# Optimization experiments

Measured on AMD Instinct MI355X. Metric: run time of the kernel, lower is better.

Reference implementation:

```python
import jax, jax.numpy as jnp
import numpy as np

B, N = 2, 1024
DIM, HEADS, DH, MLP = 768, 12, 64, 3072
PD = 768          # channels * patch_size^2 = 3*16*16
GRID = 16         # image_size // patch_size
DEPTH = 8
INNER = HEADS * DH


def layer_norm(x, g):
    # torch F.layer_norm with beta=0 buffer, eps=1e-5
    m = x.mean(-1, keepdims=True)
    v = ((x - m) ** 2).mean(-1, keepdims=True)
    return (x - m) / jnp.sqrt(v + 1e-5) * g


def qk_rmsnorm(x, g):
    # F.normalize(x, dim=-1) * sqrt(DH) * gamma ; gamma is [H,1,DH]
    n = jnp.linalg.norm(x, axis=-1, keepdims=True)
    return x / jnp.maximum(n, 1e-12) * (DH ** 0.5) * g


def setup_inputs() -> dict:
    key = jax.random.key(0)
    ks = jax.random.split(key, 16)
    s = 0.02
    d = {
        "patches": jax.random.normal(ks[0], (B, N, PD), dtype=jnp.float32),
        "h_idx": jax.random.randint(ks[1], (B, N), 0, GRID),
        "w_idx": jax.random.randint(ks[2], (B, N), 0, GRID),
        "image_ids": jnp.sort(jax.random.randint(ks[3], (B, N), 0, 8), axis=-1),
        "pos_h": jax.random.normal(ks[4], (GRID, PD)) * s,
        "pos_w": jax.random.normal(ks[5], (GRID, PD)) * s,
        "Wp": jax.random.normal(ks[6], (PD, DIM)) * s,
        "bp": jnp.zeros((DIM,)),
        "ln_p": jnp.ones((DIM,)),
        "ln1": jnp.ones((DEPTH, DIM)),
        "qg": jnp.ones((DEPTH, HEADS, 1, DH)),
        "kg": jnp.ones((DEPTH, HEADS, 1, DH)),
        "Wq": jax.random.normal(ks[7], (DEPTH, DIM, INNER)) * s,
        "Wkv": jax.random.normal(ks[8], (DEPTH, DIM, 2 * INNER)) * s,
        "Wo": jax.random.normal(ks[9], (DEPTH, INNER, DIM)) * s,
        "ln2": jnp.ones((DEPTH, DIM)),
        "W1": jax.random.normal(ks[10], (DEPTH, DIM, MLP)) * s,
        "b1": jnp.zeros((DEPTH, MLP)),
        "W2": jax.random.normal(ks[11], (DEPTH, MLP, DIM)) * s,
        "b2": jnp.zeros((DEPTH, DIM)),
        "lnf": jnp.ones((DIM,)),
    }
    return d


def reference(patches, h_idx, w_idx, image_ids, pos_h, pos_w, Wp, bp, ln_p,
              ln1, qg, kg, Wq, Wkv, Wo, ln2, W1, b1, W2, b2, lnf):
    # pos embed added to raw patches before projection (pos_embed_before_proj=True)
    x = patches + pos_h[h_idx] + pos_w[w_idx]            # [B,N,PD]
    x = layer_norm(x @ Wp + bp, ln_p)                    # [B,N,DIM]

    # block-diagonal attn_mask: tokens attend only within their own packed image
    mask = image_ids[:, None, :, None] == image_ids[:, None, None, :]  # [B,1,N,N]

    for i in range(DEPTH):
        xn = layer_norm(x, ln1[i])
        q = (xn @ Wq[i]).reshape(B, N, HEADS, DH).transpose(0, 2, 1, 3)
        k, v = jnp.split(xn @ Wkv[i], 2, axis=-1)
        k = k.reshape(B, N, HEADS, DH).transpose(0, 2, 1, 3)
        v = v.reshape(B, N, HEADS, DH).transpose(0, 2, 1, 3)
        q = qk_rmsnorm(q, qg[i])
        k = qk_rmsnorm(k, kg[i])
        dots = jnp.einsum('bhid,bhjd->bhij', q, k)       # [B,H,N,N]
        dots = jnp.where(mask, dots, -jnp.finfo(dots.dtype).max)
        attn = jax.nn.softmax(dots, axis=-1)
        o = jnp.einsum('bhij,bhjd->bhid', attn, v)
        o = o.transpose(0, 2, 1, 3).reshape(B, N, INNER)
        x = o @ Wo[i] + x
        h = jax.nn.gelu(layer_norm(x, ln2[i]) @ W1[i] + b1[i], approximate=False)
        x = (h @ W2[i] + b2[i]) + x
    return layer_norm(x, lnf)
```

## Files before the change

kernel.cpp:

```cpp
#include <hip/hip_runtime.h>
#include <hip/hip_bf16.h>
#include <math.h>

typedef _Float16 f16;
typedef f16   f16x8 __attribute__((ext_vector_type(8)));
typedef float f32x4 __attribute__((ext_vector_type(4)));
typedef unsigned short ushort_t;

#define DIM   768
#define HEADS 12
#define DH    64
#define MLP_  3072
#define NTOK  2048
#define SEQ   1024
#define WELTS 7077888

__device__ __forceinline__ ushort_t h2u(f16 h){ return __builtin_bit_cast(ushort_t, h); }
__device__ __forceinline__ unsigned pk2h(float a, float b){
  return (unsigned)h2u((f16)a) | ((unsigned)h2u((f16)b) << 16);
}
__device__ __forceinline__ void gload16(const void* g, void* l){
  __builtin_amdgcn_global_load_lds(
      (const __attribute__((address_space(1))) void*)g,
      (__attribute__((address_space(3))) void*)l, 16, 0, 0);
}
__device__ __forceinline__ float wred_sum(float v){
  #pragma unroll
  for (int o = 32; o > 0; o >>= 1) v += __shfl_xor(v, o);
  return v;
}

__global__ __launch_bounds__(256) void convert_w_kernel(
    const float* __restrict__ Wq, const float* __restrict__ Wkv,
    const float* __restrict__ Wo, const float* __restrict__ W1,
    const float* __restrict__ W2, int layer, int wp_only,
    f16* __restrict__ th)
{
  int bid = blockIdx.x;
  const float* src; int K, N; size_t ooff; int t;
  if (wp_only){ src = Wq; K = 768; N = 768; ooff = 0; t = bid; }
  else if (bid < 288) { src = Wq;  K = 768;  N = 768;  ooff = 0;       t = bid; }
  else if (bid < 864) { src = Wkv; K = 768;  N = 1536; ooff = 589824;  t = bid - 288; }
  else if (bid < 1152){ src = Wo;  K = 768;  N = 768;  ooff = 1769472; t = bid - 864; }
  else if (bid < 2304){ src = W1;  K = 768;  N = 3072; ooff = 2359296; t = bid - 1152; }
  else                { src = W2;  K = 3072; N = 768;  ooff = 4718592; t = bid - 2304; }
  if (!wp_only) src += (size_t)layer * K * N;
  int ntn = N >> 6;
  int tk = t / ntn, tn = t % ntn;
  int k0 = tk * 32, n0 = tn * 64;

  __shared__ ushort_t lh[32][66];
  int tid = threadIdx.x;
  #pragma unroll
  for (int rr = 0; rr < 2; rr++){
    int k = rr * 16 + (tid >> 4);
    int n = (tid & 15) * 4;
    float4 v = *(const float4*)(src + (size_t)(k0 + k) * N + n0 + n);
    lh[k][n+0] = h2u((f16)v.x); lh[k][n+1] = h2u((f16)v.y);
    lh[k][n+2] = h2u((f16)v.z); lh[k][n+3] = h2u((f16)v.w);
  }
  __syncthreads();
  int n = tid >> 2, kq = tid & 3;
  unsigned ph[4];
  #pragma unroll
  for (int j = 0; j < 4; j++)
    ph[j] = (unsigned)lh[kq*8 + 2*j][n] | ((unsigned)lh[kq*8 + 2*j + 1][n] << 16);
  size_t obase = ooff + (size_t)(n0 + n) * K + k0 + kq * 8;
  *(uint4*)(th + obase) = make_uint4(ph[0], ph[1], ph[2], ph[3]);
}

template<int MW>
__global__ __launch_bounds__(256) void gemm_kernel(
    const f16* __restrict__ Aq, const f16* __restrict__ Bw,
    const float* __restrict__ bias, const float* __restrict__ res,
    float* __restrict__ C, f16* __restrict__ Cq,
    f16* __restrict__ Qh, f16* __restrict__ Kt, f16* __restrict__ Vt,
    int N, int K, int nbx, int mode)
{
  constexpr int BM = MW * 32;
  __shared__ __align__(16) f16 sA[2][BM * 64];
  __shared__ __align__(16) f16 sB[2][64 * 64];
  const int tid = threadIdx.x;
  const int wid = tid >> 6, lane = tid & 63;
  constexpr int nbyl = (MW == 4) ? 4 : 5;
  const int nwg = nbx << nbyl;
  const int bid = blockIdx.x;
  const int swz = (bid & 7) * (nwg >> 3) + (bid >> 3);
  const int by = swz & ((1 << nbyl) - 1), bx = swz >> nbyl;
  const int brow = by * BM, bcol = bx << 6;
  const int m2 = wid & 1, n2 = wid >> 1;
  const int fr = lane & 15, fq = lane >> 4;
  const int Kc = K / (int)gridDim.z;
  const int kbase = (int)blockIdx.z * Kc;
  const int nk = Kc >> 6;

  const f16* pA = Aq + (size_t)brow * K + kbase;
  const f16* pB = Bw + (size_t)bcol * K + kbase;

  f32x4 acc[MW][2] = {};

  auto STAGE = [&](int buf, int ks){
    const int k0 = ks << 6;
    #pragma unroll
    for (int i = 0; i < MW; i++){
      int idx = tid + i * 256;
      int r = idx >> 3, c = idx & 7;
      int gc = c ^ (r & 7);
      gload16(pA + (size_t)r * K + k0 + gc * 8, &sA[buf][idx * 8]);
    }
    #pragma unroll
    for (int i = 0; i < 2; i++){
      int idx = tid + i * 256;
      int r = idx >> 3, c = idx & 7;
      int gc = c ^ (r & 7);
      gload16(pB + (size_t)r * K + k0 + gc * 8, &sB[buf][idx * 8]);
    }
  };

  STAGE(0, 0);
  __syncthreads();
  int cur = 0;
  for (int ks = 0; ks < nk; ks++){
    if (ks + 1 < nk) STAGE(cur ^ 1, ks + 1);
    #pragma unroll
    for (int s = 0; s < 2; s++){
      f16x8 a[MW], b[2];
      #pragma unroll
      for (int m = 0; m < MW; m++){
        int r = m2 * (MW * 16) + m * 16 + fr;
        int ch = (s * 4 + fq) ^ (r & 7);
        a[m] = *(const f16x8*)(&sA[cur][r * 64 + ch * 8]);
      }
      #pragma unroll
      for (int n = 0; n < 2; n++){
        int r = n2 * 32 + n * 16 + fr;
        int ch = (s * 4 + fq) ^ (r & 7);
        b[n] = *(const f16x8*)(&sB[cur][r * 64 + ch * 8]);
      }
      #pragma unroll
      for (int m = 0; m < MW; m++)
        #pragma unroll
        for (int n = 0; n < 2; n++)
          acc[m][n] = __builtin_amdgcn_mfma_f32_16x16x32_f16(a[m], b[n], acc[m][n], 0, 0, 0);
    }
    __syncthreads();
    cur ^= 1;
  }

  #pragma unroll
  for (int n = 0; n < 2; n++){
    int col = bcol + n2 * 32 + n * 16 + fr;
    float bv = bias ? bias[col] : 0.f;
    #pragma unroll
    for (int m = 0; m < MW; m++){
      int row0 = brow + m2 * (MW * 16) + m * 16 + (fq << 2);
      if (mode == 3){
        float* P = C + (size_t)blockIdx.z * ((size_t)NTOK * N);
        #pragma unroll
        for (int i = 0; i < 4; i++)
          P[(size_t)(row0 + i) * N + col] = acc[m][n][i];
      } else if (mode == 2){
        if (col < 768){
          #pragma unroll
          for (int i = 0; i < 4; i++)
            Qh[(size_t)(row0 + i) * 768 + col] = (f16)acc[m][n][i];
        } else if (col < 1536){
          int hcol = col - 768, hh = hcol >> 6, dd = hcol & 63;
          #pragma unroll
          for (int i = 0; i < 4; i++){
            int row = row0 + i;
            int bq = row >> 10, tok = row & 1023;
            Kt[((size_t)(bq * 12 + hh) * 1024 + tok) * 64 + dd] = (f16)acc[m][n][i];
          }
        } else {
          int hcol = col - 1536, hh = hcol >> 6, dd = hcol & 63;
          int bq = row0 >> 10, tok0 = row0 & 1023;
          ushort4 sv;
          sv.x = h2u((f16)acc[m][n][0]); sv.y = h2u((f16)acc[m][n][1]);
          sv.z = h2u((f16)acc[m][n][2]); sv.w = h2u((f16)acc[m][n][3]);
          *(ushort4*)(Vt + ((size_t)((bq * 12 + hh) * 64 + dd)) * 1024 + tok0) = sv;
        }
      } else if (mode == 1){
        #pragma unroll
        for (int i = 0; i < 4; i++){
          float v = acc[m][n][i] + bv;
          float ge = 0.5f * v * (1.f + erff(v * 0.70710678118654752f));
          Cq[(size_t)(row0 + i) * N + col] = (f16)ge;
        }
      } else {
        #pragma unroll
        for (int i = 0; i < 4; i++){
          float v = acc[m][n][i] + bv;
          size_t o = (size_t)(row0 + i) * N + col;
          if (res) v += res[o];
          C[o] = v;
        }
      }
    }
  }
}

__global__ __launch_bounds__(256) void lnred_kernel(
    float* __restrict__ x, const float* __restrict__ p, const float* __restrict__ badd,
    const float* __restrict__ g, f16* __restrict__ yq, float* __restrict__ yf)
{
  int wid = threadIdx.x >> 6, lane = threadIdx.x & 63;
  int row = blockIdx.x * 4 + wid;
  float* xr = x + (size_t)row * DIM;
  float v[12]; float s = 0.f;
  if (p){
    const float* p0 = p + (size_t)row * DIM;
    const float* p1 = p0 + (size_t)NTOK * DIM;
    #pragma unroll
    for (int d = 0; d < 12; d++){
      int c = d * 64 + lane;
      float t = xr[c] + p0[c] + p1[c] + badd[c];
      xr[c] = t; v[d] = t; s += t;
    }
  } else {
    #pragma unroll
    for (int d = 0; d < 12; d++){ v[d] = xr[d * 64 + lane]; s += v[d]; }
  }
  s = wred_sum(s);
  float mean = s * (1.f / 768.f);
  float q2 = 0.f;
  #pragma unroll
  for (int d = 0; d < 12; d++){ float t = v[d] - mean; q2 += t * t; }
  q2 = wred_sum(q2);
  float rstd = rsqrtf(q2 * (1.f / 768.f) + 1e-5f);
  size_t base = (size_t)row * DIM;
  #pragma unroll
  for (int d = 0; d < 12; d++){
    float y = (v[d] - mean) * rstd * g[d * 64 + lane];
    if (yq) yq[base + d * 64 + lane] = (f16)y;
    else    yf[base + d * 64 + lane] = y;
  }
}

__global__ __launch_bounds__(256) void rms_kernel(
    f16* __restrict__ qh, f16* __restrict__ kt,
    const float* __restrict__ qg, const float* __restrict__ kg)
{
  int wid = threadIdx.x >> 6, lane = threadIdx.x & 63;
  int id = blockIdx.x * 4 + wid;
  f16* p; const float* g;
  if (id < 24576){
    int tok = id / HEADS, h = id % HEADS;
    p = qh + (size_t)tok * DIM + h * 64; g = qg + h * 64;
  } else {
    int id2 = id - 24576;
    p = kt + (size_t)id2 * 64; g = kg + ((id2 >> 10) % 12) * 64;
  }
  float v = (float)p[lane];
  float n2 = wred_sum(v * v);
  float nn = fmaxf(sqrtf(n2), 1e-12f);
  p[lane] = (f16)(v * (8.f / nn) * g[lane]);
}

__global__ __launch_bounds__(256) void posadd_kernel(
    const float* __restrict__ patches, const int* __restrict__ hi,
    const int* __restrict__ wi, const float* __restrict__ ph,
    const float* __restrict__ pw, f16* __restrict__ oq)
{
  int idx = blockIdx.x * 256 + threadIdx.x;
  int tok = idx / 192, cv = idx % 192;
  float4 p = ((const float4*)patches)[idx];
  float4 a = *(const float4*)(ph + (size_t)hi[tok] * DIM + cv * 4);
  float4 b = *(const float4*)(pw + (size_t)wi[tok] * DIM + cv * 4);
  ushort4 o;
  o.x = h2u((f16)(p.x + a.x + b.x)); o.y = h2u((f16)(p.y + a.y + b.y));
  o.z = h2u((f16)(p.z + a.z + b.z)); o.w = h2u((f16)(p.w + a.w + b.w));
  ((ushort4*)oq)[idx] = o;
}

__global__ void seg_kernel(const int* __restrict__ ids, int2* __restrict__ segs)
{
  int i = blockIdx.x * 256 + threadIdx.x;
  int b = blockIdx.y;
  const int* row = ids + b * SEQ;
  int v = row[i];
  int lo = 0, hi = SEQ;
  while (lo < hi){ int mid = (lo + hi) >> 1; if (row[mid] <  v) lo = mid + 1; else hi = mid; }
  int s = lo;
  lo = 0; hi = SEQ;
  while (lo < hi){ int mid = (lo + hi) >> 1; if (row[mid] <= v) lo = mid + 1; else hi = mid; }
  segs[b * SEQ + i] = make_int2(s, lo);
}

__global__ __launch_bounds__(256) void attn_kernel(
    const f16* __restrict__ qh, const f16* __restrict__ ktp,
    const f16* __restrict__ vt, const int2* __restrict__ segs,
    f16* __restrict__ oq)
{
  __shared__ __align__(16) ushort_t Kq[32 * 64];
  __shared__ __align__(16) ushort_t Vl[64 * 40];

  const int tid = threadIdx.x;
  const int w = tid >> 6, lane = tid & 63;
  const int q15 = lane & 15, kg = lane >> 4;
  const int bh = blockIdx.x, b = bh / 12, h = bh % 12;
  const int qt = blockIdx.y;
  const int qrow = qt * 64 + w * 16 + q15;
  const size_t qtok = (size_t)b * SEQ + qrow;

  const f16* qp = qh + qtok * DIM + h * 64 + kg * 8;
  f16x8 qf[2];
  qf[0] = *(const f16x8*)(qp);
  qf[1] = *(const f16x8*)(qp + 32);

  const int2 se  = segs[qtok];
  const int2 se0 = segs[(size_t)b * SEQ + qt * 64];
  const int2 se1 = segs[(size_t)b * SEQ + qt * 64 + 63];
  const int klo = se0.x & ~31, khi = se1.y;

  float m = -3.0e38f, l = 0.f;
  f32x4 oacc[4] = {};

  const int krl = tid >> 3, kcl = tid & 7;
  const int kgc = kcl ^ (krl & 7);
  const f16* kbase = ktp + (size_t)bh * 1024 * 64;
  const int vd = tid >> 2, vko = (tid & 3) * 8;

  for (int kt0 = klo; kt0 < khi; kt0 += 32){
    gload16(kbase + (size_t)(kt0 + krl) * 64 + kgc * 8, Kq + tid * 8);
    {
      int ksrc = kt0 + vko;
      uint4 vv = *(const uint4*)(vt + ((size_t)bh * 64 + vd) * SEQ + ksrc);
      *(uint4*)((char*)Vl + vd * 80 + vko * 2) = vv;
    }
    __syncthreads();

    f32x4 s[2] = {};
    #pragma unroll
    for (int dh2 = 0; dh2 < 2; dh2++){
      #pragma unroll
      for (int khf = 0; khf < 2; khf++){
        int row = khf * 16 + q15;
        unsigned off = ((unsigned)row << 7) + ((unsigned)(dh2 * 4 + kg) << 4);
        off ^= (unsigned)(row & 7) << 4;
        f16x8 kf = *(const f16x8*)((const char*)Kq + off);
        s[khf] = __builtin_amdgcn_mfma_f32_16x16x32_f16(kf, qf[dh2], s[khf], 0, 0, 0);
      }
    }

    float p[8]; float tmax = -3.0e38f;
    #pragma unroll
    for (int khf = 0; khf < 2; khf++)
      #pragma unroll
      for (int i = 0; i < 4; i++){
        int key = kt0 + khf * 16 + kg * 4 + i;
        bool val = (key >= se.x) && (key < se.y);
        float sv = val ? s[khf][i] : -3.0e38f;
        p[khf * 4 + i] = sv;
        tmax = fmaxf(tmax, sv);
      }
    tmax = fmaxf(tmax, __shfl_xor(tmax, 16));
    tmax = fmaxf(tmax, __shfl_xor(tmax, 32));
    float mnew = fmaxf(m, tmax);
    float sc = __expf(m - mnew);
    float psum = 0.f;
    #pragma unroll
    for (int j = 0; j < 8; j++){
      float pv = (p[j] > -1.0e38f) ? __expf(p[j] - mnew) : 0.f;
      p[j] = pv; psum += pv;
    }
    psum += __shfl_xor(psum, 16);
    psum += __shfl_xor(psum, 32);
    l = l * sc + psum;
    m = mnew;
    #pragma unroll
    for (int dt = 0; dt < 4; dt++) oacc[dt] *= sc;

    unsigned u00 = pk2h(p[0], p[1]), u01 = pk2h(p[2], p[3]);
    unsigned u10 = pk2h(p[4], p[5]), u11 = pk2h(p[6], p[7]);
    int s0l = q15 + ((kg & 1) << 5);
    int s1l = s0l + 16;
    unsigned a0 = __shfl(u00, s0l), b0 = __shfl(u01, s0l);
    unsigned a1 = __shfl(u00, s1l), b1 = __shfl(u01, s1l);
    unsigned c0 = __shfl(u10, s0l), d0 = __shfl(u11, s0l);
    unsigned c1 = __shfl(u10, s1l), d1 = __shfl(u11, s1l);
    bool hih = kg >= 2;
    f16x8 pfrag = __builtin_bit_cast(f16x8,
        make_uint4(hih ? c0 : a0, hih ? d0 : b0, hih ? c1 : a1, hih ? d1 : b1));

    #pragma unroll
    for (int dt = 0; dt < 4; dt++){
      f16x8 vf = *(const f16x8*)((const char*)Vl + (dt * 16 + q15) * 80 + kg * 16);
      oacc[dt] = __builtin_amdgcn_mfma_f32_16x16x32_f16(vf, pfrag, oacc[dt], 0, 0, 0);
    }
    __syncthreads();
  }

  float rl = 1.f / l;
  size_t obase = qtok * DIM + h * 64;
  #pragma unroll
  for (int dt = 0; dt < 4; dt++){
    ushort4 hs;
    hs.x = h2u((f16)(oacc[dt][0] * rl)); hs.y = h2u((f16)(oacc[dt][1] * rl));
    hs.z = h2u((f16)(oacc[dt][2] * rl)); hs.w = h2u((f16)(oacc[dt][3] * rl));
    *(ushort4*)(oq + obase + dt * 16 + kg * 4) = hs;
  }
}

extern "C" void kernel_launch(void* const* d_in, const int* in_sizes, int n_in,
                              void* d_out, int out_size, void* d_ws, size_t ws_size,
                              hipStream_t stream)
{
  const float* patches   = (const float*)d_in[0];
  const int*   h_idx     = (const int*)d_in[1];
  const int*   w_idx     = (const int*)d_in[2];
  const int*   image_ids = (const int*)d_in[3];
  const float* pos_h = (const float*)d_in[4];
  const float* pos_w = (const float*)d_in[5];
  const float* Wp  = (const float*)d_in[6];
  const float* bp  = (const float*)d_in[7];
  const float* lnp = (const float*)d_in[8];
  const float* ln1 = (const float*)d_in[9];
  const float* qg  = (const float*)d_in[10];
  const float* kg  = (const float*)d_in[11];
  const float* Wq  = (const float*)d_in[12];
  const float* Wkv = (const float*)d_in[13];
  const float* Wo  = (const float*)d_in[14];
  const float* ln2 = (const float*)d_in[15];
  const float* W1  = (const float*)d_in[16];
  const float* b1  = (const float*)d_in[17];
  const float* W2  = (const float*)d_in[18];
  const float* b2  = (const float*)d_in[19];
  const float* lnf = (const float*)d_in[20];
  float* out = (float*)d_out;

  float* ws = (float*)d_ws;
  float* x    = ws;
  float* pbuf = x + NTOK * DIM;
  f16* qh  = (f16*)(pbuf + 2 * NTOK * DIM);
  f16* ktb = qh  + NTOK * DIM;
  f16* vtb = ktb + NTOK * DIM;
  f16* aAq = vtb + NTOK * DIM;
  f16* aBq = aAq + NTOK * DIM;
  f16* wth = aBq + NTOK * MLP_;
  int2* segs = (int2*)(wth + WELTS);

  seg_kernel<<<dim3(4, 2), 256, 0, stream>>>(image_ids, segs);
  posadd_kernel<<<1536, 256, 0, stream>>>(patches, h_idx, w_idx, pos_h, pos_w, aAq);
  convert_w_kernel<<<288, 256, 0, stream>>>(Wp, nullptr, nullptr, nullptr, nullptr, 0, 1, wth);
  gemm_kernel<2><<<384, 256, 0, stream>>>(
      aAq, wth, bp, nullptr, pbuf, nullptr, nullptr, nullptr, nullptr, DIM, DIM, 12, 0);
  lnred_kernel<<<NTOK / 4, 256, 0, stream>>>(pbuf, nullptr, nullptr, lnp, nullptr, x);

  for (int i = 0; i < 8; i++){
    convert_w_kernel<<<3456, 256, 0, stream>>>(Wq, Wkv, Wo, W1, W2, i, 0, wth);
    lnred_kernel<<<NTOK / 4, 256, 0, stream>>>(
        x, i ? pbuf : nullptr, i ? (b2 + (i - 1) * DIM) : nullptr,
        ln1 + i * DIM, aAq, nullptr);
    gemm_kernel<4><<<576, 256, 0, stream>>>(
        aAq, wth, nullptr, nullptr, nullptr, nullptr, qh, ktb, vtb,
        3 * DIM, DIM, 36, 2);
    rms_kernel<<<12288, 256, 0, stream>>>(qh, ktb, qg + i * DIM, kg + i * DIM);
    attn_kernel<<<dim3(24, 16), 256, 0, stream>>>(qh, ktb, vtb, segs, aAq);
    gemm_kernel<2><<<384, 256, 0, stream>>>(
        aAq, wth + 1769472, nullptr, x, x, nullptr, nullptr, nullptr, nullptr,
        DIM, DIM, 12, 0);
    lnred_kernel<<<NTOK / 4, 256, 0, stream>>>(x, nullptr, nullptr, ln2 + i * DIM, aAq, nullptr);
    gemm_kernel<4><<<768, 256, 0, stream>>>(
        aAq, wth + 2359296, b1 + i * MLP_, nullptr, nullptr, aBq, nullptr, nullptr, nullptr,
        MLP_, DIM, 48, 1);
    gemm_kernel<4><<<dim3(192, 1, 2), 256, 0, stream>>>(
        aBq, wth + 4718592, nullptr, nullptr, pbuf, nullptr, nullptr, nullptr, nullptr,
        DIM, MLP_, 12, 3);
  }
  lnred_kernel<<<NTOK / 4, 256, 0, stream>>>(x, pbuf, b2 + 7 * DIM, lnf, nullptr, out);
}
```

Measured before the change: 1.028 ms.

## Use 128x128 GEMM tiles, fuse QK RMSNorm into QKV epilogue, split-K by four

Replaces the templated GEMM with a 128x128-tile single-buffered kernel for QKV, MLP-up and MLP-down, plus a separate double-buffered 64x64 kernel for the small projections. The QK RMSNorm is folded into the QKV epilogue: a row norm is computed across the 64-wide head slice with lane shuffles, which removes the separate rms_kernel launch and its extra read and write pass. MLP-down now uses four K-partitions instead of two, so the layernorm reduction sums four partial buffers and the workspace grows. Larger tiles raise data reuse per block but drop double buffering and cut the block count, which lowers occupancy and the overlap of loads with compute.

After: 979.2 us. 1.05x faster.

```diff
diff --git a/kernel.cpp b/kernel.cpp
--- a/kernel.cpp
+++ b/kernel.cpp
@@ -69,25 +69,23 @@
   *(uint4*)(th + obase) = make_uint4(ph[0], ph[1], ph[2], ph[3]);
 }
 
-template<int MW>
-__global__ __launch_bounds__(256) void gemm_kernel(
+__global__ __launch_bounds__(256) void gemm_big(
     const f16* __restrict__ Aq, const f16* __restrict__ Bw,
-    const float* __restrict__ bias, const float* __restrict__ res,
+    const float* __restrict__ bias,
     float* __restrict__ C, f16* __restrict__ Cq,
     f16* __restrict__ Qh, f16* __restrict__ Kt, f16* __restrict__ Vt,
+    const float* __restrict__ qgam, const float* __restrict__ kgam,
     int N, int K, int nbx, int mode)
 {
-  constexpr int BM = MW * 32;
-  __shared__ __align__(16) f16 sA[2][BM * 64];
-  __shared__ __align__(16) f16 sB[2][64 * 64];
+  __shared__ __align__(16) f16 sA[128 * 64];
+  __shared__ __align__(16) f16 sB[128 * 64];
   const int tid = threadIdx.x;
   const int wid = tid >> 6, lane = tid & 63;
-  constexpr int nbyl = (MW == 4) ? 4 : 5;
-  const int nwg = nbx << nbyl;
+  const int nwg = nbx << 4;
   const int bid = blockIdx.x;
   const int swz = (bid & 7) * (nwg >> 3) + (bid >> 3);
-  const int by = swz & ((1 << nbyl) - 1), bx = swz >> nbyl;
-  const int brow = by * BM, bcol = bx << 6;
+  const int by = swz & 15, bx = swz >> 4;
+  const int brow = by << 7, bcol = bx << 7;
   const int m2 = wid & 1, n2 = wid >> 1;
   const int fr = lane & 15, fq = lane >> 4;
   const int Kc = K / (int)gridDim.z;
@@ -97,104 +95,212 @@
   const f16* pA = Aq + (size_t)brow * K + kbase;
   const f16* pB = Bw + (size_t)bcol * K + kbase;
 
-  f32x4 acc[MW][2] = {};
-
-  auto STAGE = [&](int buf, int ks){
+  f32x4 acc[4][4] = {};
+
+  for (int ks = 0; ks < nk; ks++){
     const int k0 = ks << 6;
-    #pragma unroll
-    for (int i = 0; i < MW; i++){
+    if (ks) __syncthreads();
+    #pragma unroll
+    for (int i = 0; i < 4; i++){
       int idx = tid + i * 256;
       int r = idx >> 3, c = idx & 7;
       int gc = c ^ (r & 7);
-      gload16(pA + (size_t)r * K + k0 + gc * 8, &sA[buf][idx * 8]);
-    }
-    #pragma unroll
-    for (int i = 0; i < 2; i++){
-      int idx = tid + i * 256;
-      int r = idx >> 3, c = idx & 7;
-      int gc = c ^ (r & 7);
-      gload16(pB + (size_t)r * K + k0 + gc * 8, &sB[buf][idx * 8]);
-    }
-  };
-
-  STAGE(0, 0);
-  __syncthreads();
-  int cur = 0;
-  for (int ks = 0; ks < nk; ks++){
-    if (ks + 1 < nk) STAGE(cur ^ 1, ks + 1);
+      gload16(pA + (size_t)r * K + k0 + gc * 8, &sA[idx * 8]);
+      gload16(pB + (size_t)r * K + k0 + gc * 8, &sB[idx * 8]);
+    }
+    __syncthreads();
     #pragma unroll
     for (int s = 0; s < 2; s++){
-      f16x8 a[MW], b[2];
-      #pragma unroll
-      for (int m = 0; m < MW; m++){
-        int r = m2 * (MW * 16) + m * 16 + fr;
+      f16x8 a[4], b[4];
+      #pragma unroll
+      for (int m = 0; m < 4; m++){
+        int r = m2 * 64 + m * 16 + fr;
         int ch = (s * 4 + fq) ^ (r & 7);
-        a[m] = *(const f16x8*)(&sA[cur][r * 64 + ch * 8]);
-      }
-      #pragma unroll
-      for (int n = 0; n < 2; n++){
-        int r = n2 * 32 + n * 16 + fr;
+        a[m] = *(const f16x8*)(&sA[r * 64 + ch * 8]);
+      }
+      #pragma unroll
+      for (int n = 0; n < 4; n++){
+        int r = n2 * 64 + n * 16 + fr;
         int ch = (s * 4 + fq) ^ (r & 7);
-        b[n] = *(const f16x8*)(&sB[cur][r * 64 + ch * 8]);
-      }
-      #pragma unroll
-      for (int m = 0; m < MW; m++)
-        #pragma unroll
-        for (int n = 0; n < 2; n++)
+        b[n] = *(const f16x8*)(&sB[r * 64 + ch * 8]);
+      }
+      #pragma unroll
+      for (int m = 0; m < 4; m++)
+        #pragma unroll
+        for (int n = 0; n < 4; n++)
           acc[m][n] = __builtin_amdgcn_mfma_f32_16x16x32_f16(a[m], b[n], acc[m][n], 0, 0, 0);
     }
-    __syncthreads();
-    cur ^= 1;
-  }
-
-  #pragma unroll
-  for (int n = 0; n < 2; n++){
-    int col = bcol + n2 * 32 + n * 16 + fr;
-    float bv = bias ? bias[col] : 0.f;
-    #pragma unroll
-    for (int m = 0; m < MW; m++){
-      int row0 = brow + m2 * (MW * 16) + m * 16 + (fq << 2);
-      if (mode == 3){
-        float* P = C + (size_t)blockIdx.z * ((size_t)NTOK * N);
-        #pragma unroll
-        for (int i = 0; i < 4; i++)
-          P[(size_t)(row0 + i) * N + col] = acc[m][n][i];
-      } else if (mode == 2){
-        if (col < 768){
+  }
+
+  if (mode == 2){
+    const int hbase = bcol + n2 * 64;
+    if (hbase < 768){
+      float gp[4];
+      #pragma unroll
+      for (int n = 0; n < 4; n++){
+        int col = hbase + n * 16 + fr;
+        gp[n] = qgam[col] * kgam[col];
+      }
+      #pragma unroll
+      for (int m = 0; m < 4; m++)
+        #pragma unroll
+        for (int i = 0; i < 4; i++){
+          float s = 0.f;
           #pragma unroll
-          for (int i = 0; i < 4; i++)
-            Qh[(size_t)(row0 + i) * 768 + col] = (f16)acc[m][n][i];
-        } else if (col < 1536){
-          int hcol = col - 768, hh = hcol >> 6, dd = hcol & 63;
+          for (int n = 0; n < 4; n++) s += acc[m][n][i] * acc[m][n][i];
+          s += __shfl_xor(s, 1); s += __shfl_xor(s, 2);
+          s += __shfl_xor(s, 4); s += __shfl_xor(s, 8);
+          float f = 8.f / fmaxf(sqrtf(s), 1e-12f);
+          int row = brow + m2 * 64 + m * 16 + (fq << 2) + i;
           #pragma unroll
-          for (int i = 0; i < 4; i++){
-            int row = row0 + i;
-            int bq = row >> 10, tok = row & 1023;
-            Kt[((size_t)(bq * 12 + hh) * 1024 + tok) * 64 + dd] = (f16)acc[m][n][i];
-          }
-        } else {
-          int hcol = col - 1536, hh = hcol >> 6, dd = hcol & 63;
+          for (int n = 0; n < 4; n++)
+            Qh[(size_t)row * 768 + hbase + n * 16 + fr] = (f16)(acc[m][n][i] * f * gp[n]);
+        }
+    } else if (hbase < 1536){
+      int hh = (hbase - 768) >> 6;
+      #pragma unroll
+      for (int m = 0; m < 4; m++)
+        #pragma unroll
+        for (int i = 0; i < 4; i++){
+          float s = 0.f;
+          #pragma unroll
+          for (int n = 0; n < 4; n++) s += acc[m][n][i] * acc[m][n][i];
+          s += __shfl_xor(s, 1); s += __shfl_xor(s, 2);
+          s += __shfl_xor(s, 4); s += __shfl_xor(s, 8);
+          float f = 8.f / fmaxf(sqrtf(s), 1e-12f);
+          int row = brow + m2 * 64 + m * 16 + (fq << 2) + i;
+          int bq = row >> 10, tok = row & 1023;
+          #pragma unroll
+          for (int n = 0; n < 4; n++)
+            Kt[((size_t)(bq * 12 + hh) * 1024 + tok) * 64 + n * 16 + fr]
+                = (f16)(acc[m][n][i] * f);
+        }
+    } else {
+      int hh = (hbase - 1536) >> 6;
+      #pragma unroll
+      for (int n = 0; n < 4; n++){
+        int dd = n * 16 + fr;
+        #pragma unroll
+        for (int m = 0; m < 4; m++){
+          int row0 = brow + m2 * 64 + m * 16 + (fq << 2);
           int bq = row0 >> 10, tok0 = row0 & 1023;
           ushort4 sv;
           sv.x = h2u((f16)acc[m][n][0]); sv.y = h2u((f16)acc[m][n][1]);
           sv.z = h2u((f16)acc[m][n][2]); sv.w = h2u((f16)acc[m][n][3]);
           *(ushort4*)(Vt + ((size_t)((bq * 12 + hh) * 64 + dd)) * 1024 + tok0) = sv;
         }
-      } else if (mode == 1){
+      }
+    }
+  } else if (mode == 1){
+    #pragma unroll
+    for (int n = 0; n < 4; n++){
+      int col = bcol + n2 * 64 + n * 16 + fr;
+      float bv = bias[col];
+      #pragma unroll
+      for (int m = 0; m < 4; m++){
+        int row0 = brow + m2 * 64 + m * 16 + (fq << 2);
         #pragma unroll
         for (int i = 0; i < 4; i++){
           float v = acc[m][n][i] + bv;
           float ge = 0.5f * v * (1.f + erff(v * 0.70710678118654752f));
           Cq[(size_t)(row0 + i) * N + col] = (f16)ge;
         }
-      } else {
-        #pragma unroll
-        for (int i = 0; i < 4; i++){
-          float v = acc[m][n][i] + bv;
-          size_t o = (size_t)(row0 + i) * N + col;
-          if (res) v += res[o];
-          C[o] = v;
-        }
+      }
+    }
+  } else {
+    float* P = C + (size_t)blockIdx.z * ((size_t)NTOK * N);
+    #pragma unroll
+    for (int n = 0; n < 4; n++){
+      int col = bcol + n2 * 64 + n * 16 + fr;
+      #pragma unroll
+      for (int m = 0; m < 4; m++){
+        int row0 = brow + m2 * 64 + m * 16 + (fq << 2);
+        #pragma unroll
+        for (int i = 0; i < 4; i++)
+          P[(size_t)(row0 + i) * N + col] = acc[m][n][i];
+      }
+    }
+  }
+}
+
+__global__ __launch_bounds__(256) void gemm_small(
+    const f16* __restrict__ Aq, const f16* __restrict__ Bw,
+    const float* __restrict__ bias, const float* __restrict__ res,
+    float* __restrict__ C, int N, int K, int nbx)
+{
+  __shared__ __align__(16) f16 sA[2][64 * 64];
+  __shared__ __align__(16) f16 sB[2][64 * 64];
+  const int tid = threadIdx.x;
+  const int wid = tid >> 6, lane = tid & 63;
+  const int nwg = nbx << 5;
+  const int bid = blockIdx.x;
+  const int swz = (bid & 7) * (nwg >> 3) + (bid >> 3);
+  const int by = swz & 31, bx = swz >> 5;
+  const int brow = by << 6, bcol = bx << 6;
+  const int m2 = wid & 1, n2 = wid >> 1;
+  const int fr = lane & 15, fq = lane >> 4;
+  const int nk = K >> 6;
+
+  const f16* pA = Aq + (size_t)brow * K;
+  const f16* pB = Bw + (size_t)bcol * K;
+
+  f32x4 acc[2][2] = {};
+
+  auto STAGE = [&](int buf, int ks){
+    const int k0 = ks << 6;
+    #pragma unroll
+    for (int i = 0; i < 2; i++){
+      int idx = tid + i * 256;
+      int r = idx >> 3, c = idx & 7;
+      int gc = c ^ (r & 7);
+      gload16(pA + (size_t)r * K + k0 + gc * 8, &sA[buf][idx * 8]);
+      gload16(pB + (size_t)r * K + k0 + gc * 8, &sB[buf][idx * 8]);
+    }
+  };
+
+  STAGE(0, 0);
+  __syncthreads();
+  int cur = 0;
+  for (int ks = 0; ks < nk; ks++){
+    if (ks + 1 < nk) STAGE(cur ^ 1, ks + 1);
+    #pragma unroll
+    for (int s = 0; s < 2; s++){
+      f16x8 a[2], b[2];
+      #pragma unroll
+      for (int m = 0; m < 2; m++){
+        int r = m2 * 32 + m * 16 + fr;
+        int ch = (s * 4 + fq) ^ (r & 7);
+        a[m] = *(const f16x8*)(&sA[cur][r * 64 + ch * 8]);
+      }
+      #pragma unroll
+      for (int n = 0; n < 2; n++){
+        int r = n2 * 32 + n * 16 + fr;
+        int ch = (s * 4 + fq) ^ (r & 7);
+        b[n] = *(const f16x8*)(&sB[cur][r * 64 + ch * 8]);
+      }
+      #pragma unroll
+      for (int m = 0; m < 2; m++)
+        #pragma unroll
+        for (int n = 0; n < 2; n++)
+          acc[m][n] = __builtin_amdgcn_mfma_f32_16x16x32_f16(a[m], b[n], acc[m][n], 0, 0, 0);
+    }
+    __syncthreads();
+    cur ^= 1;
+  }
+
+  #pragma unroll
+  for (int n = 0; n < 2; n++){
+    int col = bcol + n2 * 32 + n * 16 + fr;
+    float bv = bias ? bias[col] : 0.f;
+    #pragma unroll
+    for (int m = 0; m < 2; m++){
+      int row0 = brow + m2 * 32 + m * 16 + (fq << 2);
+      #pragma unroll
+      for (int i = 0; i < 4; i++){
+        float v = acc[m][n][i] + bv;
+        size_t o = (size_t)(row0 + i) * N + col;
+        if (res) v += res[o];
+        C[o] = v;
       }
     }
   }
@@ -202,19 +308,19 @@
 
 __global__ __launch_bounds__(256) void lnred_kernel(
     float* __restrict__ x, const float* __restrict__ p, const float* __restrict__ badd,
-    const float* __restrict__ g, f16* __restrict__ yq, float* __restrict__ yf)
+    int npart, const float* __restrict__ g, f16* __restrict__ yq, float* __restrict__ yf)
 {
   int wid = threadIdx.x >> 6, lane = threadIdx.x & 63;
   int row = blockIdx.x * 4 + wid;
   float* xr = x + (size_t)row * DIM;
   float v[12]; float s = 0.f;
-  if (p){
-    const float* p0 = p + (size_t)row * DIM;
-    const float* p1 = p0 + (size_t)NTOK * DIM;
+  if (npart){
     #pragma unroll
     for (int d = 0; d < 12; d++){
       int c = d * 64 + lane;
-      float t = xr[c] + p0[c] + p1[c] + badd[c];
+      float t = xr[c] + badd[c];
+      for (int j = 0; j < 4; j++)
+        t += p[(size_t)j * (NTOK * DIM) + (size_t)row * DIM + c];
       xr[c] = t; v[d] = t; s += t;
     }
   } else {
@@ -235,26 +341,6 @@
     if (yq) yq[base + d * 64 + lane] = (f16)y;
     else    yf[base + d * 64 + lane] = y;
   }
-}
-
-__global__ __launch_bounds__(256) void rms_kernel(
-    f16* __restrict__ qh, f16* __restrict__ kt,
-    const float* __restrict__ qg, const float* __restrict__ kg)
-{
-  int wid = threadIdx.x >> 6, lane = threadIdx.x & 63;
-  int id = blockIdx.x * 4 + wid;
-  f16* p; const float* g;
-  if (id < 24576){
-    int tok = id / HEADS, h = id % HEADS;
-    p = qh + (size_t)tok * DIM + h * 64; g = qg + h * 64;
-  } else {
-    int id2 = id - 24576;
-    p = kt + (size_t)id2 * 64; g = kg + ((id2 >> 10) % 12) * 64;
-  }
-  float v = (float)p[lane];
-  float n2 = wred_sum(v * v);
-  float nn = fmaxf(sqrtf(n2), 1e-12f);
-  p[lane] = (f16)(v * (8.f / nn) * g[lane]);
 }
 
 __global__ __launch_bounds__(256) void posadd_kernel(
@@ -432,7 +518,7 @@
   float* ws = (float*)d_ws;
   float* x    = ws;
   float* pbuf = x + NTOK * DIM;
-  f16* qh  = (f16*)(pbuf + 2 * NTOK * DIM);
+  f16* qh  = (f16*)(pbuf + 4 * NTOK * DIM);
   f16* ktb = qh  + NTOK * DIM;
   f16* vtb = ktb + NTOK * DIM;
   f16* aAq = vtb + NTOK * DIM;
@@ -443,30 +529,28 @@
   seg_kernel<<<dim3(4, 2), 256, 0, stream>>>(image_ids, segs);
   posadd_kernel<<<1536, 256, 0, stream>>>(patches, h_idx, w_idx, pos_h, pos_w, aAq);
   convert_w_kernel<<<288, 256, 0, stream>>>(Wp, nullptr, nullptr, nullptr, nullptr, 0, 1, wth);
-  gemm_kernel<2><<<384, 256, 0, stream>>>(
-      aAq, wth, bp, nullptr, pbuf, nullptr, nullptr, nullptr, nullptr, DIM, DIM, 12, 0);
-  lnred_kernel<<<NTOK / 4, 256, 0, stream>>>(pbuf, nullptr, nullptr, lnp, nullptr, x);
+  gemm_small<<<384, 256, 0, stream>>>(aAq, wth, bp, nullptr, pbuf, DIM, DIM, 12);
+  lnred_kernel<<<NTOK / 4, 256, 0, stream>>>(pbuf, nullptr, nullptr, 0, lnp, nullptr, x);
 
   for (int i = 0; i < 8; i++){
     convert_w_kernel<<<3456, 256, 0, stream>>>(Wq, Wkv, Wo, W1, W2, i, 0, wth);
     lnred_kernel<<<NTOK / 4, 256, 0, stream>>>(
-        x, i ? pbuf : nullptr, i ? (b2 + (i - 1) * DIM) : nullptr,
+        x, pbuf, i ? (b2 + (i - 1) * DIM) : nullptr, i ? 4 : 0,
         ln1 + i * DIM, aAq, nullptr);
-    gemm_kernel<4><<<576, 256, 0, stream>>>(
-        aAq, wth, nullptr, nullptr, nullptr, nullptr, qh, ktb, vtb,
-        3 * DIM, DIM, 36, 2);
-    rms_kernel<<<12288, 256, 0, stream>>>(qh, ktb, qg + i * DIM, kg + i * DIM);
+    gemm_big<<<288, 256, 0, stream>>>(
+        aAq, wth, nullptr, nullptr, nullptr, qh, ktb, vtb,
+        qg + i * DIM, kg + i * DIM, 3 * DIM, DIM, 18, 2);
     attn_kernel<<<dim3(24, 16), 256, 0, stream>>>(qh, ktb, vtb, segs, aAq);
-    gemm_kernel<2><<<384, 256, 0, stream>>>(
-        aAq, wth + 1769472, nullptr, x, x, nullptr, nullptr, nullptr, nullptr,
-        DIM, DIM, 12, 0);
-    lnred_kernel<<<NTOK / 4, 256, 0, stream>>>(x, nullptr, nullptr, ln2 + i * DIM, aAq, nullptr);
-    gemm_kernel<4><<<768, 256, 0, stream>>>(
-        aAq, wth + 2359296, b1 + i * MLP_, nullptr, nullptr, aBq, nullptr, nullptr, nullptr,
-        MLP_, DIM, 48, 1);
-    gemm_kernel<4><<<dim3(192, 1, 2), 256, 0, stream>>>(
-        aBq, wth + 4718592, nullptr, nullptr, pbuf, nullptr, nullptr, nullptr, nullptr,
-        DIM, MLP_, 12, 3);
-  }
-  lnred_kernel<<<NTOK / 4, 256, 0, stream>>>(x, pbuf, b2 + 7 * DIM, lnf, nullptr, out);
-}
+    gemm_small<<<384, 256, 0, stream>>>(
+        aAq, wth + 1769472, nullptr, x, x, DIM, DIM, 12);
+    lnred_kernel<<<NTOK / 4, 256, 0, stream>>>(
+        x, nullptr, nullptr, 0, ln2 + i * DIM, aAq, nullptr);
+    gemm_big<<<384, 256, 0, stream>>>(
+        aAq, wth + 2359296, b1 + i * MLP_, nullptr, aBq, nullptr, nullptr, nullptr,
+        nullptr, nullptr, MLP_, DIM, 24, 1);
+    gemm_big<<<dim3(96, 1, 4), 256, 0, stream>>>(
+        aBq, wth + 4718592, nullptr, pbuf, nullptr, nullptr, nullptr, nullptr,
+        nullptr, nullptr, DIM, MLP_, 6, 3);
+  }
+  lnred_kernel<<<NTOK / 4, 256, 0, stream>>>(x, pbuf, b2 + 7 * DIM, 4, lnf, nullptr, out);
+}
```
